# Performance work log

Measured on AMD Instinct MI355X. Metric: run time of the kernel, lower is better.

Reference implementation:

```python
import jax, jax.numpy as jnp
import numpy as np
import math

V, D, L, H, T, B = 32000, 1024, 4, 16, 2048, 1
HD = D // H
EPS = 1e-5

def _pos_encoding(T, D):
    pos = jnp.arange(T, dtype=jnp.float32)[:, None]                      # [T,1]
    div = jnp.exp(jnp.arange(0, D, 2, dtype=jnp.float32) * (-math.log(10000.0) / D))
    ang = pos * div                                                      # [T,D/2]
    pe = jnp.zeros((T, D), dtype=jnp.float32)
    pe = pe.at[:, 0::2].set(jnp.sin(ang)).at[:, 1::2].set(jnp.cos(ang))
    return pe

def _layernorm(x, g, b):
    mu = jnp.mean(x, axis=-1, keepdims=True)
    var = jnp.mean(jnp.square(x - mu), axis=-1, keepdims=True)
    return (x - mu) * jax.lax.rsqrt(var + EPS) * g + b

def setup_inputs() -> dict:
    key = jax.random.key(0)
    ks = jax.random.split(key, 16)
    s = 0.02
    inp = {
        'idx': jax.random.randint(ks[0], (B, T), 0, V),
        'embed': jax.random.normal(ks[1], (V, D), jnp.float32) * s,
        'Wq': jax.random.normal(ks[2], (L, D, D), jnp.float32) * s,
        'Wk': jax.random.normal(ks[3], (L, D, D), jnp.float32) * s,
        'Wv': jax.random.normal(ks[4], (L, D, D), jnp.float32) * s,
        'Wo': jax.random.normal(ks[5], (L, D, D), jnp.float32) * s,
        'bq': jnp.zeros((L, D), jnp.float32),
        'bk': jnp.zeros((L, D), jnp.float32),
        'bv': jnp.zeros((L, D), jnp.float32),
        'bo': jnp.zeros((L, D), jnp.float32),
        'ln1_g': jnp.ones((L, D), jnp.float32), 'ln1_b': jnp.zeros((L, D), jnp.float32),
        'ln2_g': jnp.ones((L, D), jnp.float32), 'ln2_b': jnp.zeros((L, D), jnp.float32),
        'w1': jax.random.normal(ks[6], (L, D, 4 * D), jnp.float32) * s,
        'b1': jnp.zeros((L, 4 * D), jnp.float32),
        'w2': jax.random.normal(ks[7], (L, 4 * D, D), jnp.float32) * s,
        'b2': jnp.zeros((L, D), jnp.float32),
        'lnf_g': jnp.ones((D,), jnp.float32), 'lnf_b': jnp.zeros((D,), jnp.float32),
        'head_w': jax.random.normal(ks[8], (D, V), jnp.float32) * s,
    }
    return inp

def _forward(idx, embed, Wq, Wk, Wv, Wo, bq, bk, bv, bo,
             ln1_g, ln1_b, ln2_g, ln2_b, w1, b1, w2, b2, lnf_g, lnf_b, head_w):
    Bs, Ts = idx.shape
    x = embed[idx] + _pos_encoding(Ts, embed.shape[1])[None]            # [B,T,D]
    causal = jnp.tril(jnp.ones((Ts, Ts), dtype=bool))                   # [T,T]
    scale = 1.0 / math.sqrt(HD)

    def block(x, p):
        wq, wk, wv, wo, q_b, k_b, v_b, o_b, g1, be1, g2, be2, fw1, fb1, fw2, fb2 = p
        h = _layernorm(x, g1, be1)
        q = (h @ wq + q_b).reshape(Bs, Ts, H, HD)
        k = (h @ wk + k_b).reshape(Bs, Ts, H, HD)
        v = (h @ wv + v_b).reshape(Bs, Ts, H, HD)
        att = jnp.einsum('bthd,bshd->bhts', q, k) * scale               # [B,H,T,T]
        att = jnp.where(causal, att, -jnp.inf)
        att = jax.nn.softmax(att, axis=-1)
        o = jnp.einsum('bhts,bshd->bthd', att, v).reshape(Bs, Ts, -1)
        x = x + (o @ wo + o_b)
        h2 = _layernorm(x, g2, be2)
        ff = jax.nn.gelu(h2 @ fw1 + fb1, approximate=False) @ fw2 + fb2
        x = x + ff
        return x, None

    params = (Wq, Wk, Wv, Wo, bq, bk, bv, bo, ln1_g, ln1_b, ln2_g, ln2_b, w1, b1, w2, b2)
    x, _ = jax.lax.scan(block, x, params)
    x = _layernorm(x, lnf_g, lnf_b)
    return x @ head_w                                                   # [B,T,V]

def reference(idx, embed, Wq, Wk, Wv, Wo, bq, bk, bv, bo,
              ln1_g, ln1_b, ln2_g, ln2_b, w1, b1, w2, b2, lnf_g, lnf_b, head_w):
    return _forward(idx, embed, Wq, Wk, Wv, Wo, bq, bk, bv, bo,
                    ln1_g, ln1_b, ln2_g, ln2_b, w1, b1, w2, b2, lnf_g, lnf_b, head_w)
```

## Files before the change

kernel.cpp:

```cpp
#include <hip/hip_runtime.h>
#include <cstdint>

using u16 = unsigned short;
using u32 = unsigned int;
typedef __bf16  bf16x8 __attribute__((ext_vector_type(8)));
typedef float   f32x4  __attribute__((ext_vector_type(4)));
typedef float   f32x16 __attribute__((ext_vector_type(16)));

__device__ __forceinline__ u16 f2b(float x) {
    u32 u = __builtin_bit_cast(u32, x);
    u = (u + 0x7fffu + ((u >> 16) & 1u)) >> 16;
    return (u16)u;
}

__device__ __forceinline__ f32x4 mfma16(bf16x8 a, bf16x8 b, f32x4 c) {
    return __builtin_amdgcn_mfma_f32_16x16x32_bf16(a, b, c, 0, 0, 0);
}
__device__ __forceinline__ f32x16 mfma32(bf16x8 a, bf16x8 b, f32x16 c) {
    return __builtin_amdgcn_mfma_f32_32x32x16_bf16(a, b, c, 0, 0, 0);
}

__device__ __forceinline__ void gload16(const void* g, void* lds) {
    auto gp = (__attribute__((address_space(1))) void*)(uintptr_t)g;
    auto lp = (__attribute__((address_space(3))) void*)(uintptr_t)lds;
    __builtin_amdgcn_global_load_lds(gp, lp, 16, 0, 0);
}

__device__ __forceinline__ int2 swz_bmbn(int nbm) {
    const int nwg = gridDim.x, orig = blockIdx.x;
    const int q = nwg >> 3, r = nwg & 7;
    const int xcd = orig & 7, lin = orig >> 3;
    const int id = (xcd < r ? xcd * (q + 1) : r * (q + 1) + (xcd - r) * q) + lin;
    return make_int2(id % nbm, id / nbm);
}

__global__ __launch_bounds__(512, 2) void gemm256_head_k(
    const u16* __restrict__ A, const u16* __restrict__ Bt,
    float* __restrict__ out, int M, int N, int K)
{
    __shared__ __align__(16) u16 lsA[4][256 * 32];
    __shared__ __align__(16) u16 lsB[4][256 * 32];
    const int nbm = M >> 8;
    const int2 bb = swz_bmbn(nbm);
    const int m0 = bb.x * 256, n0 = bb.y * 256;
    const int tid = threadIdx.x;
    const int w = tid >> 6, lane = tid & 63;
    const int wr = (w >> 2) * 128, wc = (w & 3) * 64;
    const int lr = lane & 15, lg = lane >> 4;
    const int rsw = (lg ^ ((lr >> 1) & 3)) * 8;

    const int trow = tid >> 2;
    const int ksw8 = ((tid & 3) ^ ((tid >> 3) & 3)) * 8;
    const u16* aA = A  + (size_t)(m0 + trow) * K + ksw8;
    const u16* aB = Bt + (size_t)(n0 + trow) * K + ksw8;
    u16* dA = &lsA[0][0] + trow * 32 + (tid & 3) * 8;
    u16* dB = &lsB[0][0] + trow * 32 + (tid & 3) * 8;

    f32x4 acc[8][4] = {};

    auto stage = [&](int h) {
        const int s = h & 3;
        const int koff = h * 32;
        gload16(aA + koff,                 dA + s * 8192);
        gload16(aA + koff + (size_t)128 * K, dA + s * 8192 + 4096);
        gload16(aB + koff,                 dB + s * 8192);
        gload16(aB + koff + (size_t)128 * K, dB + s * 8192 + 4096);
    };

    const int H = K >> 5;
    stage(0); stage(1); stage(2);
    asm volatile("s_waitcnt vmcnt(8)" ::: "memory");
    __builtin_amdgcn_s_barrier();

    for (int h = 0; h < H; ++h) {
        __builtin_amdgcn_sched_barrier(0);
        if (h + 3 < H) stage(h + 3);
        __builtin_amdgcn_sched_barrier(0);
        const int rem = H - 1 - h;
        if (rem >= 3)      asm volatile("s_waitcnt vmcnt(12)" ::: "memory");
        else if (rem == 2) asm volatile("s_waitcnt vmcnt(8)"  ::: "memory");
        else if (rem == 1) asm volatile("s_waitcnt vmcnt(4)"  ::: "memory");
        else               asm volatile("s_waitcnt vmcnt(0)"  ::: "memory");
        __builtin_amdgcn_s_barrier();
        __builtin_amdgcn_sched_barrier(0);

        const int s = h & 3;
        bf16x8 af[8], bfv[4];
#pragma unroll
        for (int m = 0; m < 8; m++)
            af[m] = *(const bf16x8*)&lsA[s][(wr + m * 16 + lr) * 32 + rsw];
#pragma unroll
        for (int n = 0; n < 4; n++)
            bfv[n] = *(const bf16x8*)&lsB[s][(wc + n * 16 + lr) * 32 + rsw];

        __builtin_amdgcn_s_setprio(1);
#pragma unroll
        for (int m = 0; m < 8; m++)
#pragma unroll
            for (int n = 0; n < 4; n++)
                acc[m][n] = mfma16(af[m], bfv[n], acc[m][n]);
        __builtin_amdgcn_s_setprio(0);

        __builtin_amdgcn_sched_barrier(0);
        __builtin_amdgcn_s_barrier();
    }

#pragma unroll
    for (int m = 0; m < 8; m++) {
        const int gr = m0 + wr + m * 16 + lg * 4;
#pragma unroll
        for (int r = 0; r < 4; r++) {
            float* orow = out + (size_t)(gr + r) * N + n0 + wc + lr;
#pragma unroll
            for (int n = 0; n < 4; n++)
                orow[n * 16] = acc[m][n][r];
        }
    }
}

template <int EPI>
__device__ __forceinline__ void gemm128(
    const u16* __restrict__ A, const u16* __restrict__ Bt,
    const float* __restrict__ bias,
    float* __restrict__ outf, u16* __restrict__ outb,
    int M, int N, int K, int bm, int bn)
{
    __shared__ u16 lsA[2][128 * 32];
    __shared__ u16 lsB[2][128 * 32];
    const int tid  = threadIdx.x;
    const int w    = tid >> 6, lane = tid & 63;
    const int lr   = lane & 15, lg = lane >> 4;
    const int m0   = bm * 128, n0 = bn * 128;
    const int wr   = (w >> 1) * 64, wc = (w & 1) * 64;
    f32x4 acc[4][4] = {};

    const int row0 = tid >> 2;
    const int ksw8 = ((lane & 3) ^ ((lane >> 3) & 3)) * 8;
    const u16* a0  = A  + (size_t)(m0 + row0) * K + ksw8;
    const u16* a1  = a0 + (size_t)64 * K;
    const u16* b0p = Bt + (size_t)(n0 + row0) * K + ksw8;
    const u16* b1p = b0p + (size_t)64 * K;
    const int rsw  = (lg ^ ((lr >> 1) & 3)) * 8;

    auto stage = [&](int buf, int ko) {
        char* la = (char*)lsA[buf] + w * 1024;
        char* lb = (char*)lsB[buf] + w * 1024;
        gload16(a0 + ko, la);
        gload16(a1 + ko, la + 4096);
        gload16(b0p + ko, lb);
        gload16(b1p + ko, lb + 4096);
    };
    auto compute = [&](int buf) {
        bf16x8 af[4], bfv[4];
#pragma unroll
        for (int i = 0; i < 4; i++)
            af[i] = *(const bf16x8*)&lsA[buf][(wr + i * 16 + lr) * 32 + rsw];
#pragma unroll
        for (int j = 0; j < 4; j++)
            bfv[j] = *(const bf16x8*)&lsB[buf][(wc + j * 16 + lr) * 32 + rsw];
#pragma unroll
        for (int i = 0; i < 4; i++)
#pragma unroll
            for (int j = 0; j < 4; j++)
                acc[i][j] = mfma16(af[i], bfv[j], acc[i][j]);
    };

    const int nk = K >> 5;
    stage(0, 0);
    __syncthreads();
    int cur = 0;
    for (int kt = 0; kt < nk - 1; ++kt) {
        stage(cur ^ 1, (kt + 1) * 32);
        compute(cur);
        __syncthreads();
        cur ^= 1;
    }
    compute(cur);

#pragma unroll
    for (int j = 0; j < 4; j++) {
        const int gc = n0 + wc + j * 16 + lr;
        const float bv = bias[gc];
#pragma unroll
        for (int i = 0; i < 4; i++) {
            const int grb = m0 + wr + i * 16 + lg * 4;
#pragma unroll
            for (int r = 0; r < 4; r++) {
                float v = acc[i][j][r] + bv;
                if constexpr (EPI == 1) v = 0.5f * v * (1.f + erff(v * 0.70710678118654752f));
                outb[(size_t)(grb + r) * N + gc] = f2b(v);
            }
        }
    }
}

template <int EPI>
__device__ __forceinline__ void gemm64(
    const u16* __restrict__ A, int lda, const u16* __restrict__ Bt, int ldb,
    const float* __restrict__ bias,
    float* __restrict__ outf, u16* __restrict__ outb,
    int M, int N, int kc, int bm, int bn)
{
    __shared__ u16 lsA[2][64 * 32];
    __shared__ u16 lsB[2][128 * 32];
    const int tid  = threadIdx.x;
    const int w    = tid >> 6, lane = tid & 63;
    const int lr   = lane & 15, lg = lane >> 4;
    const int m0   = bm * 64, n0 = bn * 128;
    const int wc   = w * 32;
    f32x4 acc[4][2] = {};

    const int row0 = tid >> 2;
    const int ksw8 = ((lane & 3) ^ ((lane >> 3) & 3)) * 8;
    const u16* a0  = A  + (size_t)(m0 + row0) * lda + ksw8;
    const u16* b0p = Bt + (size_t)(n0 + row0) * ldb + ksw8;
    const u16* b1p = b0p + (size_t)64 * ldb;
    const int rsw  = (lg ^ ((lr >> 1) & 3)) * 8;

    auto stage = [&](int buf, int ko) {
        char* la = (char*)lsA[buf] + w * 1024;
        char* lb = (char*)lsB[buf] + w * 1024;
        gload16(a0 + ko, la);
        gload16(b0p + ko, lb);
        gload16(b1p + ko, lb + 4096);
    };
    auto compute = [&](int buf) {
        bf16x8 af[4], bfv[2];
#pragma unroll
        for (int i = 0; i < 4; i++)
            af[i] = *(const bf16x8*)&lsA[buf][(i * 16 + lr) * 32 + rsw];
#pragma unroll
        for (int j = 0; j < 2; j++)
            bfv[j] = *(const bf16x8*)&lsB[buf][(wc + j * 16 + lr) * 32 + rsw];
#pragma unroll
        for (int i = 0; i < 4; i++)
#pragma unroll
            for (int j = 0; j < 2; j++)
                acc[i][j] = mfma16(af[i], bfv[j], acc[i][j]);
    };

    const int nk = kc >> 5;
    stage(0, 0);
    __syncthreads();
    int cur = 0;
    for (int kt = 0; kt < nk - 1; ++kt) {
        stage(cur ^ 1, (kt + 1) * 32);
        compute(cur);
        __syncthreads();
        cur ^= 1;
    }
    compute(cur);

#pragma unroll
    for (int j = 0; j < 2; j++) {
        const int gc = n0 + wc + j * 16 + lr;
        float bv = 0.f;
        if constexpr (EPI == 0) bv = bias[gc];
#pragma unroll
        for (int i = 0; i < 4; i++) {
            const int grb = m0 + i * 16 + lg * 4;
#pragma unroll
            for (int r = 0; r < 4; r++) {
                float v = acc[i][j][r] + bv;
                const size_t o = (size_t)(grb + r) * N + gc;
                if constexpr (EPI == 4) outf[o] = v;
                else                    outb[o] = f2b(v);
            }
        }
    }
}

__global__ __launch_bounds__(256) void gemm64_bias_k(
    const u16* A, const u16* Bt, const float* bias, u16* out, int M, int N, int K, int nbm)
{
    int2 b = swz_bmbn(nbm);
    gemm64<0>(A, K, Bt, K, bias, nullptr, out, M, N, K, b.x, b.y);
}
__global__ __launch_bounds__(256) void gemm64_splitk_k(
    const u16* A, const u16* Bt, float* pbuf, int M, int N, int K, int kc, int nbm)
{
    int2 b = swz_bmbn(nbm);
    const int s = blockIdx.y;
    gemm64<4>(A + (size_t)s * kc, K, Bt + (size_t)s * kc, K, nullptr,
              pbuf + (size_t)s * M * N, nullptr, M, N, kc, b.x, b.y);
}
__global__ __launch_bounds__(256) void gemm128_gelu_k(
    const u16* A, const u16* Bt, const float* bias, u16* out, int M, int N, int K, int nbm)
{
    int2 b = swz_bmbn(nbm);
    gemm128<1>(A, Bt, bias, nullptr, out, M, N, K, b.x, b.y);
}

__global__ __launch_bounds__(256) void reduce_ln_k(
    const float* __restrict__ pbuf, int S,
    const float* __restrict__ bias,
    float* __restrict__ x,
    const float* __restrict__ g, const float* __restrict__ bln,
    u16* __restrict__ hb)
{
    __shared__ float red[8];
    const int row = blockIdx.x, tid = threadIdx.x;
    const int w = tid >> 6, lane = tid & 63;
    const size_t base = (size_t)row * 256 + tid;
    float4 v = ((const float4*)x)[base];
    for (int s = 0; s < S; ++s) {
        const float4 p = ((const float4*)pbuf)[(size_t)s * 524288 + base];
        v.x += p.x; v.y += p.y; v.z += p.z; v.w += p.w;
    }
    const float4 bb = ((const float4*)bias)[tid];
    v.x += bb.x; v.y += bb.y; v.z += bb.z; v.w += bb.w;
    ((float4*)x)[base] = v;

    float s1 = v.x + v.y + v.z + v.w;
#pragma unroll
    for (int d = 1; d < 64; d <<= 1) s1 += __shfl_xor(s1, d);
    if (lane == 0) red[w] = s1;
    __syncthreads();
    const float mu = (red[0] + red[1] + red[2] + red[3]) * (1.f / 1024.f);
    const float d0 = v.x - mu, d1 = v.y - mu, d2 = v.z - mu, d3 = v.w - mu;
    float s2 = d0 * d0 + d1 * d1 + d2 * d2 + d3 * d3;
#pragma unroll
    for (int d = 1; d < 64; d <<= 1) s2 += __shfl_xor(s2, d);
    if (lane == 0) red[4 + w] = s2;
    __syncthreads();
    const float var = (red[4] + red[5] + red[6] + red[7]) * (1.f / 1024.f);
    const float rs = rsqrtf(var + 1e-5f);
    const float4 gv = ((const float4*)g)[tid];
    const float4 bv = ((const float4*)bln)[tid];
    u32 p0 = (u32)f2b(d0 * rs * gv.x + bv.x) | ((u32)f2b(d1 * rs * gv.y + bv.y) << 16);
    u32 p1 = (u32)f2b(d2 * rs * gv.z + bv.z) | ((u32)f2b(d3 * rs * gv.w + bv.w) << 16);
    ((uint2*)(hb + (size_t)row * 1024))[tid] = make_uint2(p0, p1);
}

__global__ __launch_bounds__(256) void flash_attn_k(
    const u16* __restrict__ qkv, const u16* __restrict__ vT, u16* __restrict__ out)
{
    constexpr int DS = 3072, T = 2048;
    __shared__ float mrg[2][64][32];
    __shared__ float msh[2][32], lsh[2][32];
    __shared__ u16   sbuf[2][32 * 68];
    const int w = threadIdx.x >> 6, lane = threadIdx.x & 63;
    const int lq = lane & 31, hi = lane >> 5;
    const int hoff = blockIdx.y * 64;
    const int pair = w >> 1, par = w & 1;
    const int qt = (pair == 0) ? blockIdx.x : 63 - blockIdx.x;
    const int q0 = qt * 32;
    const int qg = q0 + lq;

    const u16* qp = qkv + (size_t)qg * DS + hoff;
    const u16* kp = qkv + 1024 + hoff;

    bf16x8 qf[4];
#pragma unroll
    for (int d = 0; d < 4; d++)
        qf[d] = *(const bf16x8*)(qp + d * 16 + hi * 8);

    f32x16 o0 = {}, o1 = {};
    float m_r = -1e30f, l_r = 0.f;

    const int ntiles = (qt >> 1) + 1;
    for (int t = par; t < ntiles; t += 2) {
        const int kv0 = t * 64;
        f32x16 s0 = {}, s1 = {};
        {
            const u16* kb0 = kp + (size_t)(kv0 + lq) * DS + hi * 8;
            const u16* kb1 = kb0 + (size_t)32 * DS;
#pragma unroll
            for (int d = 0; d < 4; d++) {
                s0 = mfma32(*(const bf16x8*)(kb0 + d * 16), qf[d], s0);
                s1 = mfma32(*(const bf16x8*)(kb1 + d * 16), qf[d], s1);
            }
        }
        float p[32];
        float mx = -1e30f;
#pragma unroll
        for (int r = 0; r < 16; r++) {
            const int kvl = (r & 3) + 8 * (r >> 2) + 4 * hi;
            float v0 = (kv0 + kvl      <= qg) ? s0[r] * 0.125f : -1e30f;
            float v1 = (kv0 + 32 + kvl <= qg) ? s1[r] * 0.125f : -1e30f;
            p[r] = v0; p[16 + r] = v1;
            mx = fmaxf(mx, fmaxf(v0, v1));
        }
        mx = fmaxf(mx, __shfl_xor(mx, 32));
        const float mn = fmaxf(m_r, mx);
        const float alpha = __expf(m_r - mn);
        m_r = mn;
        float ls = 0.f;
#pragma unroll
        for (int i = 0; i < 32; i++) { p[i] = __expf(p[i] - mn); ls += p[i]; }
        ls += __shfl_xor(ls, 32);
        l_r = l_r * alpha + ls;
#pragma unroll
        for (int r = 0; r < 16; r++) { o0[r] *= alpha; o1[r] *= alpha; }
#pragma unroll
        for (int sub = 0; sub < 2; sub++) {
            u32 pw[8], x[8];
#pragma unroll
            for (int i = 0; i < 8; i++)
                pw[i] = (u32)f2b(p[sub * 16 + 2 * i]) | ((u32)f2b(p[sub * 16 + 2 * i + 1]) << 16);
#pragma unroll
            for (int i = 0; i < 8; i++) x[i] = __shfl_xor(pw[i], 32);
            u32 b0[4], b1[4];
            b0[0] = hi ? x[2]  : pw[0];  b0[1] = hi ? x[3]  : pw[1];
            b0[2] = hi ? pw[2] : x[0];   b0[3] = hi ? pw[3] : x[1];
            b1[0] = hi ? x[6]  : pw[4];  b1[1] = hi ? x[7]  : pw[5];
            b1[2] = hi ? pw[6] : x[4];   b1[3] = hi ? pw[7] : x[5];
            bf16x8 B0 = __builtin_bit_cast(bf16x8, *(const uint4*)b0);
            bf16x8 B1 = __builtin_bit_cast(bf16x8, *(const uint4*)b1);
            const u16* vb = vT + (size_t)(hoff + lq) * T + kv0 + sub * 32 + hi * 8;
            o0 = mfma32(*(const bf16x8*)vb, B0, o0);
            o0 = mfma32(*(const bf16x8*)(vb + 16), B1, o0);
            const u16* vb1 = vb + (size_t)32 * T;
            o1 = mfma32(*(const bf16x8*)vb1, B0, o1);
            o1 = mfma32(*(const bf16x8*)(vb1 + 16), B1, o1);
        }
    }

    __syncthreads();
    if (par == 0) {
#pragma unroll
        for (int r = 0; r < 16; r++) {
            const int d = (r & 3) + 8 * (r >> 2) + 4 * hi;
            mrg[pair][d][lq]      = o0[r];
            mrg[pair][d + 32][lq] = o1[r];
        }
        if (hi == 0) { msh[pair][lq] = m_r; lsh[pair][lq] = l_r; }
    }
    __syncthreads();
    if (par == 1) {
        const float m0v = msh[pair][lq], l0v = lsh[pair][lq];
        const float M = fmaxf(m0v, m_r);
        const float f0 = __expf(m0v - M), f1 = __expf(m_r - M);
        const float linv = 1.f / (l0v * f0 + l_r * f1);
        u32* sb = (u32*)sbuf[pair];
#pragma unroll
        for (int r = 0; r < 16; r += 2) {
            const int d = (r & 3) + 8 * (r >> 2) + 4 * hi;
            float va = (mrg[pair][d][lq] * f0 + o0[r] * f1) * linv;
            float vb = (mrg[pair][d + 1][lq] * f0 + o0[r + 1] * f1) * linv;
            sb[lq * 34 + (d >> 1)] = (u32)f2b(va) | ((u32)f2b(vb) << 16);
            float vc = (mrg[pair][d + 32][lq] * f0 + o1[r] * f1) * linv;
            float vd = (mrg[pair][d + 33][lq] * f0 + o1[r + 1] * f1) * linv;
            sb[lq * 34 + ((d + 32) >> 1)] = (u32)f2b(vc) | ((u32)f2b(vd) << 16);
        }
#pragma unroll
        for (int ps = 0; ps < 8; ps++) {
            const int row = ps * 4 + (lane >> 4);
            const uint2 v = *(const uint2*)&sbuf[pair][row * 68 + (lane & 15) * 4];
            *(uint2*)(out + (size_t)(q0 + row) * 1024 + hoff + (lane & 15) * 4) = v;
        }
    }
}

__global__ __launch_bounds__(256) void transpose_cvt_k(
    const float* __restrict__ src, u16* __restrict__ dst, int K, int N,
    long long srcLS, long long dstLS)
{
    __shared__ float tile[32][33];
    src += (size_t)blockIdx.z * srcLS;
    dst += (size_t)blockIdx.z * dstLS;
    const int n0 = blockIdx.x * 32, k0 = blockIdx.y * 32;
    const int tx = threadIdx.x & 31, ty = threadIdx.x >> 5;
#pragma unroll
    for (int r = 0; r < 32; r += 8)
        tile[ty + r][tx] = src[(size_t)(k0 + ty + r) * N + n0 + tx];
    __syncthreads();
#pragma unroll
    for (int r = 0; r < 32; r += 8)
        dst[(size_t)(n0 + ty + r) * K + k0 + tx] = f2b(tile[tx][ty + r]);
}

__global__ __launch_bounds__(256) void transpose_u16_k(
    const u16* __restrict__ src, u16* __restrict__ dst, int R, int C, int srcStride)
{
    __shared__ u16 tile[32][33];
    const int c0 = blockIdx.x * 32, r0 = blockIdx.y * 32;
    const int tx = threadIdx.x & 31, ty = threadIdx.x >> 5;
#pragma unroll
    for (int r = 0; r < 32; r += 8)
        tile[ty + r][tx] = src[(size_t)(r0 + ty + r) * srcStride + c0 + tx];
    __syncthreads();
#pragma unroll
    for (int r = 0; r < 32; r += 8)
        dst[(size_t)(c0 + ty + r) * R + r0 + tx] = tile[tx][ty + r];
}

__global__ __launch_bounds__(256) void concat_bias_k(
    const float* __restrict__ bq, const float* __restrict__ bk,
    const float* __restrict__ bv, float* __restrict__ bcat)
{
    const int l = blockIdx.y;
    const int j = blockIdx.x * 256 + threadIdx.x;
    float v;
    if (j < 1024)      v = bq[l * 1024 + j];
    else if (j < 2048) v = bk[l * 1024 + j - 1024];
    else               v = bv[l * 1024 + j - 2048];
    bcat[l * 3072 + j] = v;
}

__global__ __launch_bounds__(256) void embed_pos_k(
    const int* __restrict__ idx, const float* __restrict__ emb, float* __restrict__ x)
{
    const int t = blockIdx.x, tid = threadIdx.x;
    const int tok = idx[t];
    float4 e = ((const float4*)(emb + (size_t)tok * 1024))[tid];
    const int d0 = tid * 4;
    const float c = -0.0089944730195080f;
    const float a0 = (float)t * expf((float)d0 * c);
    const float a1 = (float)t * expf((float)(d0 + 2) * c);
    e.x += sinf(a0); e.y += cosf(a0); e.z += sinf(a1); e.w += cosf(a1);
    ((float4*)(x + (size_t)t * 1024))[tid] = e;
}

__global__ __launch_bounds__(256) void layernorm_k(
    const float* __restrict__ x, const float* __restrict__ g,
    const float* __restrict__ b, u16* __restrict__ out)
{
    __shared__ float red[8];
    const int row = blockIdx.x, tid = threadIdx.x;
    const int w = tid >> 6, lane = tid & 63;
    const float4 v = ((const float4*)(x + (size_t)row * 1024))[tid];
    float s = v.x + v.y + v.z + v.w;
#pragma unroll
    for (int d = 1; d < 64; d <<= 1) s += __shfl_xor(s, d);
    if (lane == 0) red[w] = s;
    __syncthreads();
    const float mu = (red[0] + red[1] + red[2] + red[3]) * (1.f / 1024.f);
    const float d0 = v.x - mu, d1 = v.y - mu, d2 = v.z - mu, d3 = v.w - mu;
    float s2 = d0 * d0 + d1 * d1 + d2 * d2 + d3 * d3;
#pragma unroll
    for (int d = 1; d < 64; d <<= 1) s2 += __shfl_xor(s2, d);
    if (lane == 0) red[4 + w] = s2;
    __syncthreads();
    const float var = (red[4] + red[5] + red[6] + red[7]) * (1.f / 1024.f);
    const float rs = rsqrtf(var + 1e-5f);
    const float4 gv = ((const float4*)g)[tid];
    const float4 bv = ((const float4*)b)[tid];
    u32 p0 = (u32)f2b(d0 * rs * gv.x + bv.x) | ((u32)f2b(d1 * rs * gv.y + bv.y) << 16);
    u32 p1 = (u32)f2b(d2 * rs * gv.z + bv.z) | ((u32)f2b(d3 * rs * gv.w + bv.w) << 16);
    ((uint2*)(out + (size_t)row * 1024))[tid] = make_uint2(p0, p1);
}

extern "C" void kernel_launch(void* const* d_in, const int* in_sizes, int n_in,
                              void* d_out, int out_size, void* d_ws, size_t ws_size,
                              hipStream_t stream)
{
    const int*   idx   = (const int*)  d_in[0];
    const float* embed = (const float*)d_in[1];
    const float* Wq    = (const float*)d_in[2];
    const float* Wk    = (const float*)d_in[3];
    const float* Wv    = (const float*)d_in[4];
    const float* Wo    = (const float*)d_in[5];
    const float* bq    = (const float*)d_in[6];
    const float* bk    = (const float*)d_in[7];
    const float* bv    = (const float*)d_in[8];
    const float* bo    = (const float*)d_in[9];
    const float* ln1g  = (const float*)d_in[10];
    const float* ln1b  = (const float*)d_in[11];
    const float* ln2g  = (const float*)d_in[12];
    const float* ln2b  = (const float*)d_in[13];
    const float* w1    = (const float*)d_in[14];
    const float* b1    = (const float*)d_in[15];
    const float* w2    = (const float*)d_in[16];
    const float* b2    = (const float*)d_in[17];
    const float* lnfg  = (const float*)d_in[18];
    const float* lnfb  = (const float*)d_in[19];
    const float* headw = (const float*)d_in[20];

    char* ws = (char*)d_ws;
    auto alloc = [&](size_t bytes) {
        char* p = ws;
        ws += (bytes + 255) & ~(size_t)255;
        return p;
    };
    u16*   qkvT = (u16*)alloc((size_t)4 * 3072 * 1024 * 2);
    u16*   WoT  = (u16*)alloc((size_t)4 * 1024 * 1024 * 2);
    u16*   w1T  = (u16*)alloc((size_t)4 * 1024 * 4096 * 2);
    u16*   w2T  = (u16*)alloc((size_t)4 * 1024 * 4096 * 2);
    u16*   hT   = (u16*)alloc((size_t)32000 * 1024 * 2);
    float* bcat = (float*)alloc((size_t)4 * 3072 * 4);
    float* x    = (float*)alloc((size_t)2048 * 1024 * 4);
    u16*   hb   = (u16*)alloc((size_t)2048 * 1024 * 2);
    u16*   qkvb = (u16*)alloc((size_t)2048 * 3072 * 2);
    u16*   vTb  = (u16*)alloc((size_t)2048 * 1024 * 2);
    u16*   ab   = (u16*)alloc((size_t)2048 * 1024 * 2);
    u16*   ff   = (u16*)alloc((size_t)2048 * 4096 * 2);
    float* pbuf = (float*)d_out;

    transpose_cvt_k<<<dim3(32, 32, 4),  256, 0, stream>>>(Wq, qkvT,            1024, 1024, 1048576, 3145728);
    transpose_cvt_k<<<dim3(32, 32, 4),  256, 0, stream>>>(Wk, qkvT + 1048576,  1024, 1024, 1048576, 3145728);
    transpose_cvt_k<<<dim3(32, 32, 4),  256, 0, stream>>>(Wv, qkvT + 2097152,  1024, 1024, 1048576, 3145728);
    transpose_cvt_k<<<dim3(32, 32, 4),  256, 0, stream>>>(Wo, WoT,             1024, 1024, 1048576, 1048576);
    transpose_cvt_k<<<dim3(128, 32, 4), 256, 0, stream>>>(w1, w1T,             1024, 4096, 4194304, 4194304);
    transpose_cvt_k<<<dim3(32, 128, 4), 256, 0, stream>>>(w2, w2T,             4096, 1024, 4194304, 4194304);
    transpose_cvt_k<<<dim3(1000, 32, 1), 256, 0, stream>>>(headw, hT,          1024, 32000, 0, 0);
    concat_bias_k<<<dim3(12, 4), 256, 0, stream>>>(bq, bk, bv, bcat);

    embed_pos_k<<<dim3(2048), 256, 0, stream>>>(idx, embed, x);
    layernorm_k<<<dim3(2048), 256, 0, stream>>>(x, ln1g, ln1b, hb);

    for (int l = 0; l < 4; ++l) {
        gemm64_bias_k<<<dim3(768), 256, 0, stream>>>(hb, qkvT + (size_t)l * 3145728,
                                                     bcat + l * 3072, qkvb, 2048, 3072, 1024, 32);
        transpose_u16_k<<<dim3(32, 64), 256, 0, stream>>>(qkvb + 2048, vTb, 2048, 1024, 3072);
        flash_attn_k<<<dim3(32, 16), 256, 0, stream>>>(qkvb, vTb, ab);
        gemm64_splitk_k<<<dim3(256, 2), 256, 0, stream>>>(ab, WoT + (size_t)l * 1048576,
                                                          pbuf, 2048, 1024, 1024, 512, 32);
        reduce_ln_k<<<dim3(2048), 256, 0, stream>>>(pbuf, 2, bo + l * 1024, x,
                                                    ln2g + l * 1024, ln2b + l * 1024, hb);
        gemm128_gelu_k<<<dim3(512), 256, 0, stream>>>(hb, w1T + (size_t)l * 4194304,
                                                      b1 + l * 4096, ff, 2048, 4096, 1024, 16);
        gemm64_splitk_k<<<dim3(256, 4), 256, 0, stream>>>(ff, w2T + (size_t)l * 4194304,
                                                          pbuf, 2048, 1024, 4096, 1024, 32);
        const float* ng = (l < 3) ? (ln1g + (l + 1) * 1024) : lnfg;
        const float* nb = (l < 3) ? (ln1b + (l + 1) * 1024) : lnfb;
        reduce_ln_k<<<dim3(2048), 256, 0, stream>>>(pbuf, 4, b2 + l * 1024, x, ng, nb, hb);
    }
    gemm256_head_k<<<dim3(1000), 512, 0, stream>>>(hb, hT, (float*)d_out, 2048, 32000, 1024);
}
```

Measured before the change: 1.060 ms.

## Double-buffer LDS fragment reads in head GEMM and use 128-tile QKV GEMM

Result: no change. 1.039 ms (-2.0%).

```diff
diff --git a/kernel.cpp b/kernel.cpp
--- a/kernel.cpp
+++ b/kernel.cpp
@@ -34,9 +34,10 @@
     return make_int2(id % nbm, id / nbm);
 }
 
+template <int KV>
 __global__ __launch_bounds__(512, 2) void gemm256_head_k(
     const u16* __restrict__ A, const u16* __restrict__ Bt,
-    float* __restrict__ out, int M, int N, int K)
+    float* __restrict__ out, int M, int N)
 {
     __shared__ __align__(16) u16 lsA[4][256 * 32];
     __shared__ __align__(16) u16 lsB[4][256 * 32];
@@ -51,8 +52,8 @@
 
     const int trow = tid >> 2;
     const int ksw8 = ((tid & 3) ^ ((tid >> 3) & 3)) * 8;
-    const u16* aA = A  + (size_t)(m0 + trow) * K + ksw8;
-    const u16* aB = Bt + (size_t)(n0 + trow) * K + ksw8;
+    const u16* aA = A  + (size_t)(m0 + trow) * KV + ksw8;
+    const u16* aB = Bt + (size_t)(n0 + trow) * KV + ksw8;
     u16* dA = &lsA[0][0] + trow * 32 + (tid & 3) * 8;
     u16* dB = &lsB[0][0] + trow * 32 + (tid & 3) * 8;
 
@@ -61,48 +62,55 @@
     auto stage = [&](int h) {
         const int s = h & 3;
         const int koff = h * 32;
-        gload16(aA + koff,                 dA + s * 8192);
-        gload16(aA + koff + (size_t)128 * K, dA + s * 8192 + 4096);
-        gload16(aB + koff,                 dB + s * 8192);
-        gload16(aB + koff + (size_t)128 * K, dB + s * 8192 + 4096);
-    };
-
-    const int H = K >> 5;
+        gload16(aA + koff,                    dA + s * 8192);
+        gload16(aA + koff + (size_t)128 * KV, dA + s * 8192 + 4096);
+        gload16(aB + koff,                    dB + s * 8192);
+        gload16(aB + koff + (size_t)128 * KV, dB + s * 8192 + 4096);
+    };
+
+    bf16x8 ra0[8], rb0[4], ra1[8], rb1[4];
+    auto lread = [&](bf16x8* af, bf16x8* bf, int h) {
+        const int s = h & 3;
+#pragma unroll
+        for (int m = 0; m < 8; m++)
+            af[m] = *(const bf16x8*)&lsA[s][(wr + m * 16 + lr) * 32 + rsw];
+#pragma unroll
+        for (int n = 0; n < 4; n++)
+            bf[n] = *(const bf16x8*)&lsB[s][(wc + n * 16 + lr) * 32 + rsw];
+    };
+    auto mm = [&](bf16x8* af, bf16x8* bf) {
+        __builtin_amdgcn_s_setprio(1);
+#pragma unroll
+        for (int m = 0; m < 8; m++)
+#pragma unroll
+            for (int n = 0; n < 4; n++)
+                acc[m][n] = mfma16(af[m], bf[n], acc[m][n]);
+        __builtin_amdgcn_s_setprio(0);
+    };
+    auto body = [&](int h, bf16x8* aCur, bf16x8* bCur, bf16x8* aNxt, bf16x8* bNxt) {
+        constexpr int H = KV >> 5;
+        if (h + 3 < H) stage(h + 3);
+        asm volatile("s_waitcnt lgkmcnt(0)" ::: "memory");
+        const int rem = H - 1 - h;
+        if (rem >= 3)      asm volatile("s_waitcnt vmcnt(8)" ::: "memory");
+        else if (rem == 2) asm volatile("s_waitcnt vmcnt(4)" ::: "memory");
+        else if (rem == 1) asm volatile("s_waitcnt vmcnt(0)" ::: "memory");
+        __builtin_amdgcn_s_barrier();
+        __builtin_amdgcn_sched_barrier(0);
+        if (h + 1 < H) lread(aNxt, bNxt, h + 1);
+        mm(aCur, bCur);
+    };
+
+    constexpr int H = KV >> 5;
     stage(0); stage(1); stage(2);
     asm volatile("s_waitcnt vmcnt(8)" ::: "memory");
     __builtin_amdgcn_s_barrier();
-
-    for (int h = 0; h < H; ++h) {
-        __builtin_amdgcn_sched_barrier(0);
-        if (h + 3 < H) stage(h + 3);
-        __builtin_amdgcn_sched_barrier(0);
-        const int rem = H - 1 - h;
-        if (rem >= 3)      asm volatile("s_waitcnt vmcnt(12)" ::: "memory");
-        else if (rem == 2) asm volatile("s_waitcnt vmcnt(8)"  ::: "memory");
-        else if (rem == 1) asm volatile("s_waitcnt vmcnt(4)"  ::: "memory");
-        else               asm volatile("s_waitcnt vmcnt(0)"  ::: "memory");
-        __builtin_amdgcn_s_barrier();
-        __builtin_amdgcn_sched_barrier(0);
-
-        const int s = h & 3;
-        bf16x8 af[8], bfv[4];
-#pragma unroll
-        for (int m = 0; m < 8; m++)
-            af[m] = *(const bf16x8*)&lsA[s][(wr + m * 16 + lr) * 32 + rsw];
-#pragma unroll
-        for (int n = 0; n < 4; n++)
-            bfv[n] = *(const bf16x8*)&lsB[s][(wc + n * 16 + lr) * 32 + rsw];
-
-        __builtin_amdgcn_s_setprio(1);
-#pragma unroll
-        for (int m = 0; m < 8; m++)
-#pragma unroll
-            for (int n = 0; n < 4; n++)
-                acc[m][n] = mfma16(af[m], bfv[n], acc[m][n]);
-        __builtin_amdgcn_s_setprio(0);
-
-        __builtin_amdgcn_sched_barrier(0);
-        __builtin_amdgcn_s_barrier();
+    lread(ra0, rb0, 0);
+
+#pragma unroll
+    for (int h = 0; h < H; h += 2) {
+        body(h,     ra0, rb0, ra1, rb1);
+        body(h + 1, ra1, rb1, ra0, rb0);
     }
 
 #pragma unroll
@@ -122,7 +130,7 @@
 __device__ __forceinline__ void gemm128(
     const u16* __restrict__ A, const u16* __restrict__ Bt,
     const float* __restrict__ bias,
-    float* __restrict__ outf, u16* __restrict__ outb,
+    u16* __restrict__ outb,
     int M, int N, int K, int bm, int bn)
 {
     __shared__ u16 lsA[2][128 * 32];
@@ -270,11 +278,11 @@
     }
 }
 
-__global__ __launch_bounds__(256) void gemm64_bias_k(
+__global__ __launch_bounds__(256) void gemm128_bias_k(
     const u16* A, const u16* Bt, const float* bias, u16* out, int M, int N, int K, int nbm)
 {
     int2 b = swz_bmbn(nbm);
-    gemm64<0>(A, K, Bt, K, bias, nullptr, out, M, N, K, b.x, b.y);
+    gemm128<0>(A, Bt, bias, out, M, N, K, b.x, b.y);
 }
 __global__ __launch_bounds__(256) void gemm64_splitk_k(
     const u16* A, const u16* Bt, float* pbuf, int M, int N, int K, int kc, int nbm)
@@ -288,7 +296,7 @@
     const u16* A, const u16* Bt, const float* bias, u16* out, int M, int N, int K, int nbm)
 {
     int2 b = swz_bmbn(nbm);
-    gemm128<1>(A, Bt, bias, nullptr, out, M, N, K, b.x, b.y);
+    gemm128<1>(A, Bt, bias, out, M, N, K, b.x, b.y);
 }
 
 __global__ __launch_bounds__(256) void reduce_ln_k(
@@ -600,8 +608,8 @@
     layernorm_k<<<dim3(2048), 256, 0, stream>>>(x, ln1g, ln1b, hb);
 
     for (int l = 0; l < 4; ++l) {
-        gemm64_bias_k<<<dim3(768), 256, 0, stream>>>(hb, qkvT + (size_t)l * 3145728,
-                                                     bcat + l * 3072, qkvb, 2048, 3072, 1024, 32);
+        gemm128_bias_k<<<dim3(384), 256, 0, stream>>>(hb, qkvT + (size_t)l * 3145728,
+                                                      bcat + l * 3072, qkvb, 2048, 3072, 1024, 16);
         transpose_u16_k<<<dim3(32, 64), 256, 0, stream>>>(qkvb + 2048, vTb, 2048, 1024, 3072);
         flash_attn_k<<<dim3(32, 16), 256, 0, stream>>>(qkvb, vTb, ab);
         gemm64_splitk_k<<<dim3(256, 2), 256, 0, stream>>>(ab, WoT + (size_t)l * 1048576,
@@ -616,5 +624,5 @@
         const float* nb = (l < 3) ? (ln1b + (l + 1) * 1024) : lnfb;
         reduce_ln_k<<<dim3(2048), 256, 0, stream>>>(pbuf, 4, b2 + l * 1024, x, ng, nb, hb);
     }
-    gemm256_head_k<<<dim3(1000), 512, 0, stream>>>(hb, hT, (float*)d_out, 2048, 32000, 1024);
-}
+    gemm256_head_k<1024><<<dim3(1000), 512, 0, stream>>>(hb, hT, (float*)d_out, 2048, 32000);
+}
```
